# Performance work log

Hardware: AMD Instinct MI355X
Metric: run time of the kernel (lower is better)

Reference implementation:

```python
import jax, jax.numpy as jnp
import numpy as np

B, F, D = 16384, 256, 128
H = [512, 256]
OUT = 8
VOCAB = 100000


def setup_inputs() -> dict:
    key = jax.random.key(0)
    ks = jax.random.split(key, 16)
    s = lambda k, *sh: jax.random.normal(k, sh, jnp.float32) * 0.05
    return dict(
        features=jax.random.normal(ks[0], (B, F), jnp.float32),
        ent_idx=jax.random.randint(ks[1], (B,), 0, VOCAB),
        target=jax.random.randint(ks[2], (B,), 0, OUT),
        Wf=s(ks[3], F, D), bf=jnp.zeros((D,), jnp.float32),
        Wu=s(ks[4], D, D), bu=jnp.zeros((D,), jnp.float32),
        w_cf=s(ks[5], D), w_fc=s(ks[6], D),
        w_ef=s(ks[7], D), w_fe=s(ks[8], D),
        b_c=jnp.zeros((1,), jnp.float32), b_e=jnp.zeros((1,), jnp.float32),
        head_tab=s(ks[9], VOCAB, D), ent_tab=s(ks[10], VOCAB, D),
        W0=s(ks[11], 2 * D, H[0]), b0=jnp.zeros((H[0],), jnp.float32),
        W1=s(ks[12], H[0], H[1]), b1=jnp.zeros((H[1],), jnp.float32),
        W2=s(ks[13], H[1], OUT), b2=jnp.zeros((OUT,), jnp.float32),
    )


def cross_compress(f, e, w_cf, w_fc, w_ef, w_fe, b_c, b_e):
    # torch code builds c = f (outer) e of shape (B,D,D) then matmuls a (D,1)
    # vector; algebraically (f e^T) w = f * (e . w), so we use the O(B*D) form.
    ew_cf = e @ w_cf  # (B,)
    fw_fc = f @ w_fc
    ew_ef = e @ w_ef
    fw_fe = f @ w_fe
    new_f = f * ew_cf[:, None] + e * fw_fc[:, None] + b_c
    new_e = f * ew_ef[:, None] + e * fw_fe[:, None] + b_e
    return new_f, new_e


def reference(features, ent_idx, target, Wf, bf, Wu, bu, w_cf, w_fc, w_ef,
              w_fe, b_c, b_e, head_tab, ent_tab, W0, b0, W1, b1, W2, b2):
    # 'rec' branch of CompanyOperationEvaluation.forward (eval mode, dropout=id)
    cf = jax.nn.relu(features @ Wf + bf)          # feature_layer
    e = ent_tab[ent_idx]                           # entity_embed lookup
    h = head_tab[ent_idx]                          # head_embed lookup (same ids)
    for _ in range(2):
        cf = jax.nn.relu(cf @ Wu + bu)             # user_low_mlp_layer
        h, e = cross_compress(h, e, w_cf, w_fc, w_ef, w_fe, b_c, b_e)
    high = jnp.concatenate([cf, e], axis=1)        # (B, 2D)
    x = jax.nn.relu(high @ W0 + b0)
    x = jax.nn.relu(x @ W1 + b1)
    x = jax.nn.relu(x @ W2 + b2)                   # pred_last_layer
    prob = jax.nn.softmax(x, axis=1)
    return (prob, target)
```

## Files before the change

### kernel.cpp

```cpp
#include <hip/hip_runtime.h>
#include <hip/hip_bf16.h>


typedef __bf16 bf16x8 __attribute__((ext_vector_type(8)));
typedef float floatx4 __attribute__((ext_vector_type(4)));

__device__ __forceinline__ unsigned short f2bf(float x) {
  unsigned int u = __builtin_bit_cast(unsigned int, x);
  u = (u + 0x7FFFu + ((u >> 16) & 1u)) >> 16;
  return (unsigned short)u;
}

__device__ __forceinline__ int sz(int row, int col) {
  return col ^ ((row & 7) << 3);
}

#define BAR_VM(N)                                                      \
  do {                                                                 \
    asm volatile("s_waitcnt vmcnt(" #N ") lgkmcnt(0)" ::: "memory");   \
    __builtin_amdgcn_s_barrier();                                      \
    __builtin_amdgcn_sched_barrier(0);                                 \
  } while (0)

__global__ __launch_bounds__(256) void prep_kernel(
    const float* __restrict__ Wf, const float* __restrict__ Wu,
    const float* __restrict__ W0, const float* __restrict__ W1,
    const float* __restrict__ W2,
    unsigned short* __restrict__ wfT, unsigned short* __restrict__ wuT,
    unsigned short* __restrict__ w0T, unsigned short* __restrict__ w1T,
    unsigned short* __restrict__ w2T) {
  __shared__ unsigned short tile[32][34];
  const int bid = blockIdx.x, tid = threadIdx.x;
  if (bid < 304) {
    int t = bid;
    const float* src; unsigned short* dst; int N, K, kt, nt;
    if (t < 32)       { src = Wf; dst = wfT; N = 128; K = 256; kt = t >> 2;       nt = t & 3; }
    else if (t < 48)  { t -= 32;  src = Wu; dst = wuT; N = 128; K = 128; kt = t >> 2; nt = t & 3; }
    else if (t < 176) { t -= 48;  src = W0; dst = w0T; N = 512; K = 256; kt = t >> 4; nt = t & 15; }
    else              { t -= 176; src = W1; dst = w1T; N = 256; K = 512; kt = t >> 3; nt = t & 7; }
    {
      int r = tid >> 3, cg = (tid & 7) * 4;
      float4 v = *(const float4*)(src + (size_t)(kt * 32 + r) * N + nt * 32 + cg);
      tile[r][cg + 0] = f2bf(v.x); tile[r][cg + 1] = f2bf(v.y);
      tile[r][cg + 2] = f2bf(v.z); tile[r][cg + 3] = f2bf(v.w);
    }
    __syncthreads();
    {
      int rp = tid >> 3, cg = (tid & 7) * 4;
      uint2 o;
      o.x = (unsigned)tile[cg + 0][rp] | ((unsigned)tile[cg + 1][rp] << 16);
      o.y = (unsigned)tile[cg + 2][rp] | ((unsigned)tile[cg + 3][rp] << 16);
      *(uint2*)(dst + (size_t)(nt * 32 + rp) * K + kt * 32 + cg) = o;
    }
  } else {
#pragma unroll
    for (int i = 0; i < 8; ++i) {
      int g = tid * 8 + i, k = g >> 3, n = g & 7;
      w2T[n * 256 + k] = f2bf(W2[g]);
    }
  }
}

template <int LDK>
__device__ __forceinline__ void stageB(unsigned short* dstbase,
                                       const unsigned short* __restrict__ src,
                                       int tid) {
#pragma unroll
  for (int i = 0; i < 4; ++i) {
    int chunk = i * 512 + tid;
    int row = chunk >> 4, seg = chunk & 15;
    int segl = seg ^ (row & 7);
    const unsigned short* g = src + (size_t)row * LDK + segl * 8;
    unsigned short* d = dstbase + chunk * 8;
    __builtin_amdgcn_global_load_lds((const unsigned int*)g, (unsigned int*)d,
                                     16, 0, 0);
  }
}

template <int PASS, int LDK>
__device__ __forceinline__ const unsigned short* srcstep(
    const unsigned short* __restrict__ s, int st) {
  return s + (size_t)(st / PASS) * 128 * LDK + (st % PASS) * 128;
}

template <int LDA>
__device__ __forceinline__ void mstep(const unsigned short* A,
                                      const unsigned short* bt, int k0,
                                      floatx4* acc, int m16, int quad,
                                      int wm, int wn) {
#pragma unroll
  for (int kk = 0; kk < 128; kk += 32) {
    const int ca = k0 + kk + quad * 8;
    const int cb = kk + quad * 8;
    const int ra0 = wm * 32 + m16, ra1 = wm * 32 + 16 + m16;
    const int rb0 = wn * 32 + m16, rb1 = wn * 32 + 16 + m16;
    bf16x8 a0 = *(const bf16x8*)&A[ra0 * LDA + sz(ra0, ca)];
    bf16x8 a1 = *(const bf16x8*)&A[ra1 * LDA + sz(ra1, ca)];
    bf16x8 b0 = *(const bf16x8*)&bt[rb0 * 128 + sz(rb0, cb)];
    bf16x8 b1 = *(const bf16x8*)&bt[rb1 * 128 + sz(rb1, cb)];
    acc[0] = __builtin_amdgcn_mfma_f32_16x16x32_bf16(a0, b0, acc[0], 0, 0, 0);
    acc[1] = __builtin_amdgcn_mfma_f32_16x16x32_bf16(a0, b1, acc[1], 0, 0, 0);
    acc[2] = __builtin_amdgcn_mfma_f32_16x16x32_bf16(a1, b0, acc[2], 0, 0, 0);
    acc[3] = __builtin_amdgcn_mfma_f32_16x16x32_bf16(a1, b1, acc[3], 0, 0, 0);
  }
}

template <int T, int LDA, int PASS, int LDK>
__device__ __forceinline__ void gemm_phase(
    const unsigned short* A, const unsigned short* __restrict__ src,
    unsigned short* b_sh, floatx4* acc, int tid, int m16, int quad, int wm,
    int wn) {
  stageB<LDK>(b_sh, srcstep<PASS, LDK>(src, 0), tid);
  if (T > 1) {
    stageB<LDK>(b_sh + 16384, srcstep<PASS, LDK>(src, 1), tid);
    BAR_VM(4);
  } else {
    BAR_VM(0);
  }
#pragma unroll
  for (int t = 0; t < T; ++t) {
    if (t + 2 < T)
      stageB<LDK>(b_sh + ((t + 2) % 3) * 16384, srcstep<PASS, LDK>(src, t + 2),
                  tid);
    mstep<LDA>(A, b_sh + (t % 3) * 16384, (t % PASS) * 128,
               acc + (t / PASS) * 4, m16, quad, wm, wn);
    if (t + 2 < T) {
      BAR_VM(4);
    } else {
      BAR_VM(0);
    }
  }
}

__global__ __launch_bounds__(512, 2) void fused_mlp_kernel(
    const float* __restrict__ features, const int* __restrict__ ent_idx,
    const float* __restrict__ head_tab, const float* __restrict__ ent_tab,
    const float* __restrict__ w_cf, const float* __restrict__ w_fc,
    const float* __restrict__ w_ef, const float* __restrict__ w_fe,
    const float* __restrict__ b_c, const float* __restrict__ b_e,
    const unsigned short* __restrict__ wfT,
    const unsigned short* __restrict__ wuT, const float* __restrict__ bf_,
    const float* __restrict__ bu,
    const unsigned short* __restrict__ w0T, const float* __restrict__ b0,
    const unsigned short* __restrict__ w1T, const float* __restrict__ b1,
    const unsigned short* __restrict__ w2T, const float* __restrict__ b2,
    const int* __restrict__ target, float* __restrict__ out) {
  __shared__ __align__(16) unsigned short regionA[32768];
  __shared__ __align__(16) unsigned short b_sh[3 * 16384];
  unsigned short* feat_sh = regionA;
  unsigned short* buf0 = regionA + 16384;
  unsigned short* buf1 = regionA + 24576;
  unsigned short* A_sh = regionA;
  unsigned short* x0_sh = regionA;
  unsigned short* x1_sh = b_sh;

  const int tid = threadIdx.x;
  const int r0 = blockIdx.x * 64;
  const int lane = tid & 63, wave = tid >> 6;
  const int m16 = lane & 15, quad = lane >> 4;
  const int wm = wave >> 2, wn = wave & 3;

  const int grow = tid >> 3, gpart = tid & 7;
  const int gidx = ent_idx[r0 + grow];
  const float* hp = head_tab + (size_t)gidx * 128 + gpart * 16;
  const float* ep = ent_tab + (size_t)gidx * 128 + gpart * 16;
  float4 h4[4], e4[4];
#pragma unroll
  for (int j = 0; j < 4; ++j) {
    h4[j] = *(const float4*)(hp + j * 4);
    e4[j] = *(const float4*)(ep + j * 4);
  }

#pragma unroll
  for (int i = 0; i < 8; ++i) {
    int idx4 = i * 512 + tid;
    int row = idx4 >> 6, c = (idx4 & 63) * 4;
    float4 v = *(const float4*)(features + (size_t)(r0 + row) * 256 + c);
    uint2 o;
    o.x = (unsigned)f2bf(v.x) | ((unsigned)f2bf(v.y) << 16);
    o.y = (unsigned)f2bf(v.z) | ((unsigned)f2bf(v.w) << 16);
    *(uint2*)&feat_sh[row * 256 + sz(row, c)] = o;
  }

  floatx4 acc[4];
#pragma unroll
  for (int j = 0; j < 4; ++j) acc[j] = (floatx4){0.f, 0.f, 0.f, 0.f};
  gemm_phase<2, 256, 2, 256>(feat_sh, wfT, b_sh, acc, tid, m16, quad, wm, wn);
#pragma unroll
  for (int mi = 0; mi < 2; ++mi)
#pragma unroll
    for (int ni = 0; ni < 2; ++ni) {
      int col = wn * 32 + ni * 16 + m16;
      float bv = bf_[col];
#pragma unroll
      for (int r = 0; r < 4; ++r) {
        int row = wm * 32 + mi * 16 + quad * 4 + r;
        buf0[row * 128 + sz(row, col)] =
            f2bf(fmaxf(acc[mi * 2 + ni][r] + bv, 0.f));
      }
    }

  {
    float h[16], e[16];
#pragma unroll
    for (int j = 0; j < 4; ++j) {
      h[4 * j + 0] = h4[j].x; h[4 * j + 1] = h4[j].y;
      h[4 * j + 2] = h4[j].z; h[4 * j + 3] = h4[j].w;
      e[4 * j + 0] = e4[j].x; e[4 * j + 1] = e4[j].y;
      e[4 * j + 2] = e4[j].z; e[4 * j + 3] = e4[j].w;
    }
    float wcf[16], wfc[16], wef[16], wfe[16];
#pragma unroll
    for (int jj = 0; jj < 4; ++jj) {
      *(float4*)&wcf[jj * 4] = *(const float4*)(w_cf + gpart * 16 + jj * 4);
      *(float4*)&wfc[jj * 4] = *(const float4*)(w_fc + gpart * 16 + jj * 4);
      *(float4*)&wef[jj * 4] = *(const float4*)(w_ef + gpart * 16 + jj * 4);
      *(float4*)&wfe[jj * 4] = *(const float4*)(w_fe + gpart * 16 + jj * 4);
    }
    const float bc = b_c[0], be = b_e[0];
#pragma unroll
    for (int it = 0; it < 2; ++it) {
      float d0 = 0.f, d1 = 0.f, d2 = 0.f, d3 = 0.f;
#pragma unroll
      for (int j = 0; j < 16; ++j) {
        d0 += e[j] * wcf[j]; d1 += h[j] * wfc[j];
        d2 += e[j] * wef[j]; d3 += h[j] * wfe[j];
      }
#pragma unroll
      for (int s = 1; s < 8; s <<= 1) {
        d0 += __shfl_xor(d0, s); d1 += __shfl_xor(d1, s);
        d2 += __shfl_xor(d2, s); d3 += __shfl_xor(d3, s);
      }
#pragma unroll
      for (int j = 0; j < 16; ++j) {
        float nh = h[j] * d0 + e[j] * d1 + bc;
        float ne = h[j] * d2 + e[j] * d3 + be;
        h[j] = nh; e[j] = ne;
      }
    }
    uint4 o0, o1;
    unsigned* w = (unsigned*)&o0;
#pragma unroll
    for (int j = 0; j < 4; ++j)
      w[j] = (unsigned)f2bf(e[2 * j]) | ((unsigned)f2bf(e[2 * j + 1]) << 16);
    w = (unsigned*)&o1;
#pragma unroll
    for (int j = 0; j < 4; ++j)
      w[j] = (unsigned)f2bf(e[8 + 2 * j]) |
             ((unsigned)f2bf(e[8 + 2 * j + 1]) << 16);
    const int c0 = 128 + gpart * 16;
    *(uint4*)&A_sh[grow * 256 + sz(grow, c0)] = o0;
    *(uint4*)&A_sh[grow * 256 + sz(grow, c0 + 8)] = o1;
  }

#pragma unroll
  for (int j = 0; j < 4; ++j) acc[j] = (floatx4){0.f, 0.f, 0.f, 0.f};
  gemm_phase<1, 128, 1, 128>(buf0, wuT, b_sh, acc, tid, m16, quad, wm, wn);
#pragma unroll
  for (int mi = 0; mi < 2; ++mi)
#pragma unroll
    for (int ni = 0; ni < 2; ++ni) {
      int col = wn * 32 + ni * 16 + m16;
      float bv = bu[col];
#pragma unroll
      for (int r = 0; r < 4; ++r) {
        int row = wm * 32 + mi * 16 + quad * 4 + r;
        buf1[row * 128 + sz(row, col)] =
            f2bf(fmaxf(acc[mi * 2 + ni][r] + bv, 0.f));
      }
    }

#pragma unroll
  for (int j = 0; j < 4; ++j) acc[j] = (floatx4){0.f, 0.f, 0.f, 0.f};
  BAR_VM(0);
  mstep<128>(buf1, b_sh, 0, acc, m16, quad, wm, wn);
  BAR_VM(0);
#pragma unroll
  for (int mi = 0; mi < 2; ++mi)
#pragma unroll
    for (int ni = 0; ni < 2; ++ni) {
      int col = wn * 32 + ni * 16 + m16;
      float bv = bu[col];
#pragma unroll
      for (int r = 0; r < 4; ++r) {
        int row = wm * 32 + mi * 16 + quad * 4 + r;
        A_sh[row * 256 + sz(row, col)] =
            f2bf(fmaxf(acc[mi * 2 + ni][r] + bv, 0.f));
      }
    }

  floatx4 acc16[16];
#pragma unroll
  for (int j = 0; j < 16; ++j) acc16[j] = (floatx4){0.f, 0.f, 0.f, 0.f};
  gemm_phase<8, 256, 2, 256>(A_sh, w0T, b_sh, acc16, tid, m16, quad, wm, wn);
#pragma unroll
  for (int np = 0; np < 4; ++np)
#pragma unroll
    for (int mi = 0; mi < 2; ++mi)
#pragma unroll
      for (int ni = 0; ni < 2; ++ni) {
        int col = np * 128 + wn * 32 + ni * 16 + m16;
        float bv = b0[col];
#pragma unroll
        for (int r = 0; r < 4; ++r) {
          int row = wm * 32 + mi * 16 + quad * 4 + r;
          x0_sh[row * 512 + sz(row, col)] =
              f2bf(fmaxf(acc16[np * 4 + mi * 2 + ni][r] + bv, 0.f));
        }
      }

  floatx4 acc8[8];
#pragma unroll
  for (int j = 0; j < 8; ++j) acc8[j] = (floatx4){0.f, 0.f, 0.f, 0.f};
  gemm_phase<8, 512, 4, 512>(x0_sh, w1T, b_sh, acc8, tid, m16, quad, wm, wn);
#pragma unroll
  for (int np = 0; np < 2; ++np)
#pragma unroll
    for (int mi = 0; mi < 2; ++mi)
#pragma unroll
      for (int ni = 0; ni < 2; ++ni) {
        int col = np * 128 + wn * 32 + ni * 16 + m16;
        float bv = b1[col];
#pragma unroll
        for (int r = 0; r < 4; ++r)
          x1_sh[(wm * 32 + mi * 16 + quad * 4 + r) * 264 + col] =
              f2bf(fmaxf(acc8[np * 4 + mi * 2 + ni][r] + bv, 0.f));
      }
  BAR_VM(0);

  {
    int row = tid >> 3, q = tid & 7;
    float p[8];
#pragma unroll
    for (int n = 0; n < 8; ++n) p[n] = 0.f;
#pragma unroll
    for (int jb = 0; jb < 4; ++jb) {
      bf16x8 xv = *(const bf16x8*)&x1_sh[row * 264 + q * 32 + jb * 8];
#pragma unroll
      for (int n = 0; n < 8; ++n) {
        bf16x8 wv = *(const bf16x8*)(w2T + n * 256 + q * 32 + jb * 8);
#pragma unroll
        for (int j = 0; j < 8; ++j) p[n] += (float)xv[j] * (float)wv[j];
      }
    }
#pragma unroll
    for (int s = 1; s < 8; s <<= 1)
#pragma unroll
      for (int n = 0; n < 8; ++n) p[n] += __shfl_xor(p[n], s);
    if (q == 0) {
      float mx = -1e30f;
#pragma unroll
      for (int n = 0; n < 8; ++n) {
        p[n] = fmaxf(p[n] + b2[n], 0.f);
        mx = fmaxf(mx, p[n]);
      }
      float sum = 0.f;
#pragma unroll
      for (int n = 0; n < 8; ++n) { p[n] = __expf(p[n] - mx); sum += p[n]; }
      const float inv = 1.f / sum;
      const int gr = r0 + row;
      float4 o0 = {p[0] * inv, p[1] * inv, p[2] * inv, p[3] * inv};
      float4 o1 = {p[4] * inv, p[5] * inv, p[6] * inv, p[7] * inv};
      *(float4*)(out + (size_t)gr * 8) = o0;
      *(float4*)(out + (size_t)gr * 8 + 4) = o1;
      out[16384 * 8 + gr] = (float)target[gr];
    }
  }
}

extern "C" void kernel_launch(void* const* d_in, const int* in_sizes, int n_in,
                              void* d_out, int out_size, void* d_ws, size_t ws_size,
                              hipStream_t stream) {
  const float* features = (const float*)d_in[0];
  const int* ent_idx    = (const int*)d_in[1];
  const int* target     = (const int*)d_in[2];
  const float* Wf  = (const float*)d_in[3];
  const float* bf_ = (const float*)d_in[4];
  const float* Wu  = (const float*)d_in[5];
  const float* bu  = (const float*)d_in[6];
  const float* w_cf = (const float*)d_in[7];
  const float* w_fc = (const float*)d_in[8];
  const float* w_ef = (const float*)d_in[9];
  const float* w_fe = (const float*)d_in[10];
  const float* b_c  = (const float*)d_in[11];
  const float* b_e  = (const float*)d_in[12];
  const float* head_tab = (const float*)d_in[13];
  const float* ent_tab  = (const float*)d_in[14];
  const float* W0 = (const float*)d_in[15];
  const float* b0 = (const float*)d_in[16];
  const float* W1 = (const float*)d_in[17];
  const float* b1 = (const float*)d_in[18];
  const float* W2 = (const float*)d_in[19];
  const float* b2 = (const float*)d_in[20];
  float* out = (float*)d_out;

  unsigned short* ws = (unsigned short*)d_ws;
  size_t off = 0;
  auto alloc = [&](size_t n) { unsigned short* p = ws + off; off += n; return p; };
  unsigned short* wfT  = alloc(32768);
  unsigned short* wuT  = alloc(16384);
  unsigned short* w0T  = alloc(131072);
  unsigned short* w1T  = alloc(131072);
  unsigned short* w2T  = alloc(2048);
  (void)ws_size; (void)in_sizes; (void)n_in; (void)out_size;

  prep_kernel<<<305, 256, 0, stream>>>(Wf, Wu, W0, W1, W2,
                                       wfT, wuT, w0T, w1T, w2T);
  fused_mlp_kernel<<<256, 512, 0, stream>>>(features, ent_idx, head_tab,
      ent_tab, w_cf, w_fc, w_ef, w_fe, b_c, b_e, wfT, wuT, bf_, bu,
      w0T, b0, w1T, b1, w2T, b2, target, out);
}
```

Baseline: 182.2 us.

## Swap MFMA operands for vectorized epilogue stores and widen N tiles for big GEMMs

MFMA operands are swapped so each lane's accumulator holds four consecutive output columns of one row. Every epilogue can then load the bias as a float4 and write packed bf16 pairs with a single 8-byte LDS store instead of four scalar stores. The two large hidden-layer GEMMs now use a wider per-wave N tile (64 columns, 8 accumulators per step) with BK=64 staging, which reuses each A fragment across more MFMAs and cuts A-side LDS reads. Feature loading is also widened to 8 elements per thread. The risks are higher register pressure under the 512x2 launch bounds and possible LDS bank conflicts from the new swizzle pattern on 64-wide rows.

```diff
diff --git a/kernel.cpp b/kernel.cpp
--- a/kernel.cpp
+++ b/kernel.cpp
@@ -9,6 +9,10 @@
   unsigned int u = __builtin_bit_cast(unsigned int, x);
   u = (u + 0x7FFFu + ((u >> 16) & 1u)) >> 16;
   return (unsigned short)u;
+}
+
+__device__ __forceinline__ unsigned pack2(float a, float b) {
+  return (unsigned)f2bf(a) | ((unsigned)f2bf(b) << 16);
 }
 
 __device__ __forceinline__ int sz(int row, int col) {
@@ -61,14 +65,14 @@
   }
 }
 
-template <int LDK>
+template <int CPR, int LDK>
 __device__ __forceinline__ void stageB(unsigned short* dstbase,
                                        const unsigned short* __restrict__ src,
                                        int tid) {
 #pragma unroll
   for (int i = 0; i < 4; ++i) {
     int chunk = i * 512 + tid;
-    int row = chunk >> 4, seg = chunk & 15;
+    int row = chunk / CPR, seg = chunk % CPR;
     int segl = seg ^ (row & 7);
     const unsigned short* g = src + (size_t)row * LDK + segl * 8;
     unsigned short* d = dstbase + chunk * 8;
@@ -77,17 +81,17 @@
   }
 }
 
-template <int PASS, int LDK>
+template <int PASS, int BK, int NROWS, int LDK>
 __device__ __forceinline__ const unsigned short* srcstep(
     const unsigned short* __restrict__ s, int st) {
-  return s + (size_t)(st / PASS) * 128 * LDK + (st % PASS) * 128;
+  return s + (size_t)(st / PASS) * NROWS * LDK + (st % PASS) * BK;
 }
 
 template <int LDA>
-__device__ __forceinline__ void mstep(const unsigned short* A,
-                                      const unsigned short* bt, int k0,
-                                      floatx4* acc, int m16, int quad,
-                                      int wm, int wn) {
+__device__ __forceinline__ void mstep_n(const unsigned short* A,
+                                        const unsigned short* bt, int k0,
+                                        floatx4* acc, int m16, int quad,
+                                        int wm, int wn) {
 #pragma unroll
   for (int kk = 0; kk < 128; kk += 32) {
     const int ca = k0 + kk + quad * 8;
@@ -98,21 +102,47 @@
     bf16x8 a1 = *(const bf16x8*)&A[ra1 * LDA + sz(ra1, ca)];
     bf16x8 b0 = *(const bf16x8*)&bt[rb0 * 128 + sz(rb0, cb)];
     bf16x8 b1 = *(const bf16x8*)&bt[rb1 * 128 + sz(rb1, cb)];
-    acc[0] = __builtin_amdgcn_mfma_f32_16x16x32_bf16(a0, b0, acc[0], 0, 0, 0);
-    acc[1] = __builtin_amdgcn_mfma_f32_16x16x32_bf16(a0, b1, acc[1], 0, 0, 0);
-    acc[2] = __builtin_amdgcn_mfma_f32_16x16x32_bf16(a1, b0, acc[2], 0, 0, 0);
-    acc[3] = __builtin_amdgcn_mfma_f32_16x16x32_bf16(a1, b1, acc[3], 0, 0, 0);
+    acc[0] = __builtin_amdgcn_mfma_f32_16x16x32_bf16(b0, a0, acc[0], 0, 0, 0);
+    acc[1] = __builtin_amdgcn_mfma_f32_16x16x32_bf16(b1, a0, acc[1], 0, 0, 0);
+    acc[2] = __builtin_amdgcn_mfma_f32_16x16x32_bf16(b0, a1, acc[2], 0, 0, 0);
+    acc[3] = __builtin_amdgcn_mfma_f32_16x16x32_bf16(b1, a1, acc[3], 0, 0, 0);
+  }
+}
+
+template <int LDA>
+__device__ __forceinline__ void mstep_w(const unsigned short* A,
+                                        const unsigned short* bt, int k0,
+                                        floatx4* acc, int m16, int quad,
+                                        int wm, int wn) {
+#pragma unroll
+  for (int kk = 0; kk < 64; kk += 32) {
+    const int ca = k0 + kk + quad * 8;
+    const int cb = kk + quad * 8;
+    const int ra0 = wm * 32 + m16, ra1 = wm * 32 + 16 + m16;
+    bf16x8 a0 = *(const bf16x8*)&A[ra0 * LDA + sz(ra0, ca)];
+    bf16x8 a1 = *(const bf16x8*)&A[ra1 * LDA + sz(ra1, ca)];
+    bf16x8 b[4];
+#pragma unroll
+    for (int ni = 0; ni < 4; ++ni) {
+      int rb = wn * 64 + ni * 16 + m16;
+      b[ni] = *(const bf16x8*)&bt[rb * 64 + sz(rb, cb)];
+    }
+#pragma unroll
+    for (int ni = 0; ni < 4; ++ni) {
+      acc[ni] = __builtin_amdgcn_mfma_f32_16x16x32_bf16(b[ni], a0, acc[ni], 0, 0, 0);
+      acc[4 + ni] = __builtin_amdgcn_mfma_f32_16x16x32_bf16(b[ni], a1, acc[4 + ni], 0, 0, 0);
+    }
   }
 }
 
 template <int T, int LDA, int PASS, int LDK>
-__device__ __forceinline__ void gemm_phase(
+__device__ __forceinline__ void gemm_phase_n(
     const unsigned short* A, const unsigned short* __restrict__ src,
     unsigned short* b_sh, floatx4* acc, int tid, int m16, int quad, int wm,
     int wn) {
-  stageB<LDK>(b_sh, srcstep<PASS, LDK>(src, 0), tid);
+  stageB<16, LDK>(b_sh, srcstep<PASS, 128, 128, LDK>(src, 0), tid);
   if (T > 1) {
-    stageB<LDK>(b_sh + 16384, srcstep<PASS, LDK>(src, 1), tid);
+    stageB<16, LDK>(b_sh + 16384, srcstep<PASS, 128, 128, LDK>(src, 1), tid);
     BAR_VM(4);
   } else {
     BAR_VM(0);
@@ -120,10 +150,37 @@
 #pragma unroll
   for (int t = 0; t < T; ++t) {
     if (t + 2 < T)
-      stageB<LDK>(b_sh + ((t + 2) % 3) * 16384, srcstep<PASS, LDK>(src, t + 2),
-                  tid);
-    mstep<LDA>(A, b_sh + (t % 3) * 16384, (t % PASS) * 128,
-               acc + (t / PASS) * 4, m16, quad, wm, wn);
+      stageB<16, LDK>(b_sh + ((t + 2) % 3) * 16384,
+                      srcstep<PASS, 128, 128, LDK>(src, t + 2), tid);
+    mstep_n<LDA>(A, b_sh + (t % 3) * 16384, (t % PASS) * 128,
+                 acc + (t / PASS) * 4, m16, quad, wm, wn);
+    if (t + 2 < T) {
+      BAR_VM(4);
+    } else {
+      BAR_VM(0);
+    }
+  }
+}
+
+template <int T, int LDA, int PASS, int LDK>
+__device__ __forceinline__ void gemm_phase_w(
+    const unsigned short* A, const unsigned short* __restrict__ src,
+    unsigned short* b_sh, floatx4* acc, int tid, int m16, int quad, int wm,
+    int wn) {
+  stageB<8, LDK>(b_sh, srcstep<PASS, 64, 256, LDK>(src, 0), tid);
+  if (T > 1) {
+    stageB<8, LDK>(b_sh + 16384, srcstep<PASS, 64, 256, LDK>(src, 1), tid);
+    BAR_VM(4);
+  } else {
+    BAR_VM(0);
+  }
+#pragma unroll
+  for (int t = 0; t < T; ++t) {
+    if (t + 2 < T)
+      stageB<8, LDK>(b_sh + ((t + 2) % 3) * 16384,
+                     srcstep<PASS, 64, 256, LDK>(src, t + 2), tid);
+    mstep_w<LDA>(A, b_sh + (t % 3) * 16384, (t % PASS) * 64,
+                 acc + (t / PASS) * 8, m16, quad, wm, wn);
     if (t + 2 < T) {
       BAR_VM(4);
     } else {
@@ -159,6 +216,8 @@
   const int lane = tid & 63, wave = tid >> 6;
   const int m16 = lane & 15, quad = lane >> 4;
   const int wm = wave >> 2, wn = wave & 3;
+  const int wn2 = wave & 1;
+  (void)wn2;
 
   const int grow = tid >> 3, gpart = tid & 7;
   const int gidx = ent_idx[r0 + grow];
@@ -172,32 +231,33 @@
   }
 
 #pragma unroll
-  for (int i = 0; i < 8; ++i) {
-    int idx4 = i * 512 + tid;
-    int row = idx4 >> 6, c = (idx4 & 63) * 4;
-    float4 v = *(const float4*)(features + (size_t)(r0 + row) * 256 + c);
-    uint2 o;
-    o.x = (unsigned)f2bf(v.x) | ((unsigned)f2bf(v.y) << 16);
-    o.y = (unsigned)f2bf(v.z) | ((unsigned)f2bf(v.w) << 16);
-    *(uint2*)&feat_sh[row * 256 + sz(row, c)] = o;
+  for (int i = 0; i < 4; ++i) {
+    int chunk = i * 512 + tid;
+    int row = chunk >> 5, c8 = (chunk & 31) * 8;
+    float4 v0 = *(const float4*)(features + (size_t)(r0 + row) * 256 + c8);
+    float4 v1 = *(const float4*)(features + (size_t)(r0 + row) * 256 + c8 + 4);
+    uint4 o;
+    o.x = pack2(v0.x, v0.y); o.y = pack2(v0.z, v0.w);
+    o.z = pack2(v1.x, v1.y); o.w = pack2(v1.z, v1.w);
+    *(uint4*)&feat_sh[row * 256 + sz(row, c8)] = o;
   }
 
   floatx4 acc[4];
 #pragma unroll
   for (int j = 0; j < 4; ++j) acc[j] = (floatx4){0.f, 0.f, 0.f, 0.f};
-  gemm_phase<2, 256, 2, 256>(feat_sh, wfT, b_sh, acc, tid, m16, quad, wm, wn);
+  gemm_phase_n<2, 256, 2, 256>(feat_sh, wfT, b_sh, acc, tid, m16, quad, wm, wn);
 #pragma unroll
   for (int mi = 0; mi < 2; ++mi)
 #pragma unroll
     for (int ni = 0; ni < 2; ++ni) {
-      int col = wn * 32 + ni * 16 + m16;
-      float bv = bf_[col];
-#pragma unroll
-      for (int r = 0; r < 4; ++r) {
-        int row = wm * 32 + mi * 16 + quad * 4 + r;
-        buf0[row * 128 + sz(row, col)] =
-            f2bf(fmaxf(acc[mi * 2 + ni][r] + bv, 0.f));
-      }
+      int row = wm * 32 + mi * 16 + m16;
+      int col = wn * 32 + ni * 16 + quad * 4;
+      float4 bv = *(const float4*)(bf_ + col);
+      floatx4 v = acc[mi * 2 + ni];
+      uint2 o;
+      o.x = pack2(fmaxf(v[0] + bv.x, 0.f), fmaxf(v[1] + bv.y, 0.f));
+      o.y = pack2(fmaxf(v[2] + bv.z, 0.f), fmaxf(v[3] + bv.w, 0.f));
+      *(uint2*)&buf0[row * 128 + sz(row, col)] = o;
     }
 
   {
@@ -241,13 +301,10 @@
     uint4 o0, o1;
     unsigned* w = (unsigned*)&o0;
 #pragma unroll
-    for (int j = 0; j < 4; ++j)
-      w[j] = (unsigned)f2bf(e[2 * j]) | ((unsigned)f2bf(e[2 * j + 1]) << 16);
+    for (int j = 0; j < 4; ++j) w[j] = pack2(e[2 * j], e[2 * j + 1]);
     w = (unsigned*)&o1;
 #pragma unroll
-    for (int j = 0; j < 4; ++j)
-      w[j] = (unsigned)f2bf(e[8 + 2 * j]) |
-             ((unsigned)f2bf(e[8 + 2 * j + 1]) << 16);
+    for (int j = 0; j < 4; ++j) w[j] = pack2(e[8 + 2 * j], e[8 + 2 * j + 1]);
     const int c0 = 128 + gpart * 16;
     *(uint4*)&A_sh[grow * 256 + sz(grow, c0)] = o0;
     *(uint4*)&A_sh[grow * 256 + sz(grow, c0 + 8)] = o1;
@@ -255,77 +312,77 @@
 
 #pragma unroll
   for (int j = 0; j < 4; ++j) acc[j] = (floatx4){0.f, 0.f, 0.f, 0.f};
-  gemm_phase<1, 128, 1, 128>(buf0, wuT, b_sh, acc, tid, m16, quad, wm, wn);
+  gemm_phase_n<1, 128, 1, 128>(buf0, wuT, b_sh, acc, tid, m16, quad, wm, wn);
 #pragma unroll
   for (int mi = 0; mi < 2; ++mi)
 #pragma unroll
     for (int ni = 0; ni < 2; ++ni) {
-      int col = wn * 32 + ni * 16 + m16;
-      float bv = bu[col];
-#pragma unroll
-      for (int r = 0; r < 4; ++r) {
-        int row = wm * 32 + mi * 16 + quad * 4 + r;
-        buf1[row * 128 + sz(row, col)] =
-            f2bf(fmaxf(acc[mi * 2 + ni][r] + bv, 0.f));
-      }
+      int row = wm * 32 + mi * 16 + m16;
+      int col = wn * 32 + ni * 16 + quad * 4;
+      float4 bv = *(const float4*)(bu + col);
+      floatx4 v = acc[mi * 2 + ni];
+      uint2 o;
+      o.x = pack2(fmaxf(v[0] + bv.x, 0.f), fmaxf(v[1] + bv.y, 0.f));
+      o.y = pack2(fmaxf(v[2] + bv.z, 0.f), fmaxf(v[3] + bv.w, 0.f));
+      *(uint2*)&buf1[row * 128 + sz(row, col)] = o;
     }
 
 #pragma unroll
   for (int j = 0; j < 4; ++j) acc[j] = (floatx4){0.f, 0.f, 0.f, 0.f};
   BAR_VM(0);
-  mstep<128>(buf1, b_sh, 0, acc, m16, quad, wm, wn);
+  mstep_n<128>(buf1, b_sh, 0, acc, m16, quad, wm, wn);
   BAR_VM(0);
 #pragma unroll
   for (int mi = 0; mi < 2; ++mi)
 #pragma unroll
     for (int ni = 0; ni < 2; ++ni) {
-      int col = wn * 32 + ni * 16 + m16;
-      float bv = bu[col];
-#pragma unroll
-      for (int r = 0; r < 4; ++r) {
-        int row = wm * 32 + mi * 16 + quad * 4 + r;
-        A_sh[row * 256 + sz(row, col)] =
-            f2bf(fmaxf(acc[mi * 2 + ni][r] + bv, 0.f));
-      }
+      int row = wm * 32 + mi * 16 + m16;
+      int col = wn * 32 + ni * 16 + quad * 4;
+      float4 bv = *(const float4*)(bu + col);
+      floatx4 v = acc[mi * 2 + ni];
+      uint2 o;
+      o.x = pack2(fmaxf(v[0] + bv.x, 0.f), fmaxf(v[1] + bv.y, 0.f));
+      o.y = pack2(fmaxf(v[2] + bv.z, 0.f), fmaxf(v[3] + bv.w, 0.f));
+      *(uint2*)&A_sh[row * 256 + sz(row, col)] = o;
     }
 
   floatx4 acc16[16];
 #pragma unroll
   for (int j = 0; j < 16; ++j) acc16[j] = (floatx4){0.f, 0.f, 0.f, 0.f};
-  gemm_phase<8, 256, 2, 256>(A_sh, w0T, b_sh, acc16, tid, m16, quad, wm, wn);
-#pragma unroll
-  for (int np = 0; np < 4; ++np)
+  gemm_phase_w<8, 256, 4, 256>(A_sh, w0T, b_sh, acc16, tid, m16, quad, wm, wn);
+#pragma unroll
+  for (int np = 0; np < 2; ++np)
 #pragma unroll
     for (int mi = 0; mi < 2; ++mi)
 #pragma unroll
-      for (int ni = 0; ni < 2; ++ni) {
-        int col = np * 128 + wn * 32 + ni * 16 + m16;
-        float bv = b0[col];
-#pragma unroll
-        for (int r = 0; r < 4; ++r) {
-          int row = wm * 32 + mi * 16 + quad * 4 + r;
-          x0_sh[row * 512 + sz(row, col)] =
-              f2bf(fmaxf(acc16[np * 4 + mi * 2 + ni][r] + bv, 0.f));
-        }
+      for (int ni = 0; ni < 4; ++ni) {
+        int row = wm * 32 + mi * 16 + m16;
+        int col = np * 256 + wn * 64 + ni * 16 + quad * 4;
+        float4 bv = *(const float4*)(b0 + col);
+        floatx4 v = acc16[np * 8 + mi * 4 + ni];
+        uint2 o;
+        o.x = pack2(fmaxf(v[0] + bv.x, 0.f), fmaxf(v[1] + bv.y, 0.f));
+        o.y = pack2(fmaxf(v[2] + bv.z, 0.f), fmaxf(v[3] + bv.w, 0.f));
+        *(uint2*)&x0_sh[row * 512 + sz(row, col)] = o;
       }
 
   floatx4 acc8[8];
 #pragma unroll
   for (int j = 0; j < 8; ++j) acc8[j] = (floatx4){0.f, 0.f, 0.f, 0.f};
-  gemm_phase<8, 512, 4, 512>(x0_sh, w1T, b_sh, acc8, tid, m16, quad, wm, wn);
-#pragma unroll
-  for (int np = 0; np < 2; ++np)
-#pragma unroll
-    for (int mi = 0; mi < 2; ++mi)
-#pragma unroll
-      for (int ni = 0; ni < 2; ++ni) {
-        int col = np * 128 + wn * 32 + ni * 16 + m16;
-        float bv = b1[col];
-#pragma unroll
-        for (int r = 0; r < 4; ++r)
-          x1_sh[(wm * 32 + mi * 16 + quad * 4 + r) * 264 + col] =
-              f2bf(fmaxf(acc8[np * 4 + mi * 2 + ni][r] + bv, 0.f));
-      }
+  gemm_phase_w<8, 512, 8, 512>(x0_sh, w1T, b_sh, acc8, tid, m16, quad, wm, wn);
+#pragma unroll
+  for (int mi = 0; mi < 2; ++mi)
+#pragma unroll
+    for (int ni = 0; ni < 4; ++ni) {
+      int row = wm * 32 + mi * 16 + m16;
+      int col = wn * 64 + ni * 16 + quad * 4;
+      float4 bv = *(const float4*)(b1 + col);
+      floatx4 v = acc8[mi * 4 + ni];
+      uint2 o;
+      o.x = pack2(fmaxf(v[0] + bv.x, 0.f), fmaxf(v[1] + bv.y, 0.f));
+      o.y = pack2(fmaxf(v[2] + bv.z, 0.f), fmaxf(v[3] + bv.w, 0.f));
+      *(uint2*)&x1_sh[row * 264 + col] = o;
+    }
   BAR_VM(0);
 
   {
```

Result: no change. 179.5 us (-1.5%).
